# Optimization experiments

Measured on AMD Instinct MI355X. Metric: run time of the kernel, lower is better.

The kernel has to match this reference:

```python
import jax, jax.numpy as jnp
import numpy as np

B, L, D = 32, 2048, 512
MODES = 32
H = 1           # num_head
E = D // H      # per-head channels
KMA = 128       # moving_avg kernel
EPS = 1e-5


def setup_inputs() -> dict:
    key = jax.random.key(0)
    ks = jax.random.split(key, 12)
    scale = 1.0 / (D * D)
    lin = lambda k, fi, fo: jax.random.uniform(k, (fo, fi), jnp.float32, -1, 1) / np.sqrt(fi)
    return {
        "x": jax.random.normal(ks[0], (B, L, D), jnp.float32),
        "W_in": lin(ks[1], D, H * E),
        "b_in": jnp.zeros((H * E,), jnp.float32),
        "Wf_r": scale * jax.random.uniform(ks[2], (H, E, E, MODES), jnp.float32),
        "Wf_i": scale * jax.random.uniform(ks[3], (H, E, E, MODES), jnp.float32),
        "W_out": lin(ks[4], H * E, D),
        "b_out": jnp.zeros((D,), jnp.float32),
        "W_conv1": lin(ks[5], D, D),
        "W_conv2": lin(ks[6], D, D),
        "bn_gamma": jnp.ones((L,), jnp.float32),
        "bn_beta": jnp.zeros((L,), jnp.float32),
    }


def moving_average(x, k):
    # x: (b, l, c); replicate-pad front/end exactly as the torch module, then avg-pool k/stride 1
    front = jnp.repeat(x[:, :1, :], k - 1 - (k - 1) // 2, axis=1)
    end = jnp.repeat(x[:, -1:, :], (k - 1) // 2, axis=1)
    xp = jnp.concatenate([front, x, end], axis=1)          # (b, l+k-1, c)
    cs = jnp.cumsum(xp, axis=1)
    cs = jnp.concatenate([jnp.zeros_like(cs[:, :1]), cs], axis=1)
    return (cs[:, k:] - cs[:, :-k]) / k                    # (b, l, c)


def reference(x, W_in, b_in, Wf_r, Wf_i, W_out, b_out, W_conv1, W_conv2, bn_gamma, bn_beta):
    b, l, d = x.shape
    # in projection -> (b, l, h, e) -> (b, h, e, l)
    q = x @ W_in.T + b_in
    q = q.reshape(b, l, H, E).transpose(0, 2, 3, 1)
    # FourierBlock: rfft over time, keep lowest MODES modes, complex mix, irfft
    x_ft = jnp.fft.rfft(q, axis=-1)                        # (b, h, e, l//2+1)
    Wf = (Wf_r + 1j * Wf_i).astype(x_ft.dtype)             # (h, e, e, m)
    out_modes = jnp.einsum('bhim,hiom->bhom', x_ft[..., :MODES], Wf)
    out_ft = jnp.pad(out_modes, ((0, 0), (0, 0), (0, 0), (0, l // 2 + 1 - MODES)))
    fre = jnp.fft.irfft(out_ft, n=l, axis=-1)              # (b, h, e, l)
    # (b, h, e, l) -> (b, l, h*e), out projection (dropout is eval-mode identity)
    fre = fre.transpose(0, 3, 1, 2).reshape(b, l, H * E)
    fre = fre @ W_out.T + b_out
    xr = x + fre
    # series decomposition 1: keep residual
    xr = xr - moving_average(xr, KMA)
    # conv1x1 -> gelu -> conv1x1 (exact erf gelu, matching F.gelu default)
    y = jax.nn.gelu(jnp.einsum('bld,ed->ble', xr, W_conv1), approximate=False)
    y = jnp.einsum('bld,ed->ble', y, W_conv2)
    res = xr + y
    # BatchNorm1d(in_len): channel axis is the time axis, batch stats over (b, d)
    mean = res.mean(axis=(0, 2), keepdims=True)
    var = ((res - mean) ** 2).mean(axis=(0, 2), keepdims=True)
    out = bn_gamma[None, :, None] * (res - mean) / jnp.sqrt(var + EPS) + bn_beta[None, :, None]
    return out
```

## Files before the change

### kernel.cpp

```cpp
#include <hip/hip_runtime.h>
#include <hip/hip_bf16.h>
#include <math.h>

#define B_   32
#define L_   2048
#define D_   512
#define BLROWS (B_*L_)
#define NBIG ((size_t)BLROWS * D_)

typedef __hip_bfloat16 bf16;
using bf16x8 = __attribute__((ext_vector_type(8))) short;
using f32x4  = __attribute__((ext_vector_type(4))) float;

__device__ __forceinline__ unsigned short f2b(float f) {
  bf16 h = __float2bfloat16(f);
  return *reinterpret_cast<unsigned short*>(&h);
}
__device__ __forceinline__ float b2f(unsigned short u) {
  union { unsigned int i; float f; } c;
  c.i = ((unsigned int)u) << 16;
  return c.f;
}

__device__ __forceinline__ void gl_lds16(const void* g, void* l) {
  __builtin_amdgcn_global_load_lds(
      (const __attribute__((address_space(1))) void*)g,
      (__attribute__((address_space(3))) void*)l, 16, 0, 0);
}

__global__ __launch_bounds__(256) void f2bfK(const float4* __restrict__ src,
                                             ushort4* __restrict__ dst,
                                             size_t n4) {
  for (size_t i = (size_t)blockIdx.x * 256 + threadIdx.x; i < n4;
       i += (size_t)gridDim.x * 256) {
    float4 v = src[i];
    ushort4 o;
    o.x = f2b(v.x); o.y = f2b(v.y); o.z = f2b(v.z); o.w = f2b(v.w);
    dst[i] = o;
  }
}

__global__ __launch_bounds__(256) void genTwP(float* __restrict__ TwP) {
  int idx = blockIdx.x * 256 + threadIdx.x;
  int l = idx >> 6, rem = idx & 63, mg = rem >> 4, j = rem & 15;
  int m = mg * 8 + (j & 7);
  int r = (m * l) & (L_ - 1);
  float ang = (float)r * (6.283185307179586f / (float)L_);
  TwP[idx] = (j < 8) ? cosf(ang) : -sinf(ang);
}

__global__ __launch_bounds__(256) void genTbF(float* __restrict__ Tb) {
  int idx = blockIdx.x * 256 + threadIdx.x;
  int l = idx >> 6, j = idx & 63;
  int m = j >> 1;
  int r = (m * l) & (L_ - 1);
  float ang = (float)r * (6.283185307179586f / (float)L_);
  Tb[idx] = (j & 1) ? sinf(ang) : cosf(ang);
}

__global__ __launch_bounds__(256) void genTbDbf(const float* __restrict__ Tb,
                                                bf16* __restrict__ TbD) {
  int idx = blockIdx.x * 256 + threadIdx.x;
  int l = idx >> 6, j = idx & 63;
  float s = 0.f;
  for (int t = l - 64; t < l + 64; t++) {
    int cl = min(max(t, 0), L_ - 1);
    s += Tb[cl * 64 + j];
  }
  TbD[idx] = __float2bfloat16(Tb[idx] - s * (1.f / 128.f));
}

__global__ __launch_bounds__(256) void twWf2(const float* __restrict__ Wfr,
                                             const float* __restrict__ Wfi,
                                             bf16* __restrict__ Wcat2) {
  __shared__ __align__(16) bf16 st[256 * 72];
  const int t = threadIdx.x;
  const int i0 = blockIdx.x * 64, o0 = blockIdx.y * 8;
  const int arr = blockIdx.z;
  const float* src = arr ? Wfi : Wfr;
#pragma unroll
  for (int s8 = 0; s8 < 8; s8++) {
    unsigned short v[8];
#pragma unroll
    for (int ss = 0; ss < 8; ss++)
      v[ss] = f2b(src[(size_t)(i0 + s8 * 8 + ss) * 16384 + o0 * 32 + t]);
    int4 wv;
    wv.x = (int)v[0] | ((int)v[1] << 16);
    wv.y = (int)v[2] | ((int)v[3] << 16);
    wv.z = (int)v[4] | ((int)v[5] << 16);
    wv.w = (int)v[6] | ((int)v[7] << 16);
    *(int4*)&st[t * 72 + s8 * 8] = wv;
  }
  __syncthreads();
#pragma unroll
  for (int p = 0; p < 8; p++) {
    const int om = p * 32 + (t >> 3), c = t & 7;
    const int o = om >> 5, m = om & 31;
    int4 rv = *(const int4*)&st[om * 72 + c * 8];
    bf16* dst = Wcat2 + (size_t)m * 524288 + (size_t)(o0 + o) * 1024 +
                arr * 512 + i0 + c * 8;
    *(int4*)dst = rv;
  }
}

template <bool GELU, bool RESID, bool BIAS, bool OUTBF, bool RESBF, bool AFP32>
__global__ __launch_bounds__(256) void gemm_k64(
    const void* __restrict__ Av, const bf16* __restrict__ Wt,
    const float* __restrict__ bias, const void* __restrict__ resid,
    void* __restrict__ Cout, int M, int N, int K) {
  __shared__ __align__(16) bf16 As[2][128 * 64];
  __shared__ __align__(16) bf16 Bs[2][128 * 64];
  const int t = threadIdx.x;
  const int lane = t & 63;
  const int w = t >> 6, wr = w >> 1, wc = w & 1;

  const int id = blockIdx.x;
  const int xcd = id & 7, rest = id >> 3;
  const int cb = rest & 3, rg = rest >> 2;
  const int row0 = (rg * 8 + xcd) * 128, col0 = cb * 128;

  const bf16* Ab = (const bf16*)Av;
  const float* Af = (const float*)Av;

  f32x4 acc[4][4];
#pragma unroll
  for (int i = 0; i < 4; i++)
#pragma unroll
    for (int j = 0; j < 4; j++) acc[i][j] = (f32x4){0.f, 0.f, 0.f, 0.f};

  auto stage = [&](int buf, int k0) {
#pragma unroll
    for (int s = 0; s < 4; s++) {
      const int ci = s * 256 + t;
      const int row = ci >> 3;
      const int cg = ci & 7;
      const int pc = cg ^ (row & 7);
      if (AFP32) {
        const float* ax = Af + (size_t)(row0 + row) * K + k0 + cg * 8;
        float4 v0 = *(const float4*)(ax);
        float4 v1 = *(const float4*)(ax + 4);
        int4 wv;
        wv.x = (int)f2b(v0.x) | ((int)f2b(v0.y) << 16);
        wv.y = (int)f2b(v0.z) | ((int)f2b(v0.w) << 16);
        wv.z = (int)f2b(v1.x) | ((int)f2b(v1.y) << 16);
        wv.w = (int)f2b(v1.z) | ((int)f2b(v1.w) << 16);
        *(int4*)&As[buf][(size_t)(row * 8 + pc) * 8] = wv;
      } else {
        const int kqg = cg ^ (row & 7);
        bf16* dA = &As[buf][(size_t)(s * 256 + (t & ~63)) * 8];
        gl_lds16(Ab + (size_t)(row0 + row) * K + k0 + kqg * 8, dA);
      }
      {
        const int kqg = cg ^ (row & 7);
        bf16* dB = &Bs[buf][(size_t)(s * 256 + (t & ~63)) * 8];
        gl_lds16(Wt + (size_t)(col0 + row) * K + k0 + kqg * 8, dB);
      }
    }
  };

  stage(0, 0);
  int cur = 0;
  for (int k0 = 0; k0 < K; k0 += 64) {
    __syncthreads();
    if (k0 + 64 < K) stage(cur ^ 1, k0 + 64);
#pragma unroll
    for (int ks = 0; ks < 2; ks++) {
      const int c = ks * 4 + (lane >> 4);
      const int pc = c ^ (lane & 7);
      bf16x8 af[4], bg[4];
#pragma unroll
      for (int m = 0; m < 4; m++) {
        const int ra = wr * 64 + m * 16 + (lane & 15);
        af[m] = *reinterpret_cast<const bf16x8*>(&As[cur][(ra * 8 + pc) * 8]);
      }
#pragma unroll
      for (int n = 0; n < 4; n++) {
        const int rb = wc * 64 + n * 16 + (lane & 15);
        bg[n] = *reinterpret_cast<const bf16x8*>(&Bs[cur][(rb * 8 + pc) * 8]);
      }
#pragma unroll
      for (int n = 0; n < 4; n++)
#pragma unroll
        for (int m = 0; m < 4; m++)
          acc[n][m] = __builtin_amdgcn_mfma_f32_16x16x32_bf16(
              bg[n], af[m], acc[n][m], 0, 0, 0);
    }
    cur ^= 1;
  }

  float* Cf = (float*)Cout;
  ushort* Cb = (ushort*)Cout;
#pragma unroll
  for (int n = 0; n < 4; n++) {
    const int dbase = col0 + wc * 64 + n * 16 + ((lane >> 4) << 2);
    float4 bsv = {0.f, 0.f, 0.f, 0.f};
    if (BIAS) bsv = *(const float4*)(bias + dbase);
#pragma unroll
    for (int m = 0; m < 4; m++) {
      const size_t r = (size_t)row0 + wr * 64 + m * 16 + (lane & 15);
      float v[4];
#pragma unroll
      for (int j = 0; j < 4; j++) {
        float u = acc[n][m][j] + (BIAS ? (&bsv.x)[j] : 0.f);
        if (GELU) u = 0.5f * u * (1.0f + erff(u * 0.70710678118654752f));
        v[j] = u;
      }
      if (RESID) {
        if (RESBF) {
          ushort4 rv = *(const ushort4*)((const ushort*)resid + r * N + dbase);
          v[0] += b2f(rv.x); v[1] += b2f(rv.y);
          v[2] += b2f(rv.z); v[3] += b2f(rv.w);
        } else {
          float4 rv = *(const float4*)((const float*)resid + r * N + dbase);
          v[0] += rv.x; v[1] += rv.y; v[2] += rv.z; v[3] += rv.w;
        }
      }
      if (OUTBF) {
        ushort4 o = {f2b(v[0]), f2b(v[1]), f2b(v[2]), f2b(v[3])};
        *(ushort4*)(Cb + r * N + dbase) = o;
      } else {
        float4 o = {v[0], v[1], v[2], v[3]};
        *(float4*)(Cf + r * N + dbase) = o;
      }
    }
  }
}

__global__ __launch_bounds__(256) void gemmD(
    const bf16* __restrict__ TbD, const bf16* __restrict__ CCT,
    const ushort* __restrict__ u, ushort* __restrict__ xr) {
  __shared__ __align__(16) bf16 As[128 * 64];
  __shared__ __align__(16) bf16 Bs[128 * 64];
  const int t = threadIdx.x;
  const int lane = t & 63;
  const int wid = t >> 6, wr = wid >> 1, wc = wid & 1;
  const int row0 = blockIdx.x * 128, col0 = blockIdx.y * 128;
  const int b = blockIdx.z;
  const bf16* Bsrc = CCT + (size_t)b * 512 * 64;

  const int srow = t >> 3, schk = t & 7;
  const int wb16 = (t & ~63) * 8;
#pragma unroll
  for (int p = 0; p < 4; p++) {
    gl_lds16(TbD + (size_t)(row0 + srow + 32 * p) * 64 + schk * 8,
             &As[p * 2048 + wb16]);
    gl_lds16(Bsrc + (size_t)(col0 + srow + 32 * p) * 64 + schk * 8,
             &Bs[p * 2048 + wb16]);
  }
  __syncthreads();

  f32x4 acc[4][4];
#pragma unroll
  for (int i = 0; i < 4; i++)
#pragma unroll
    for (int j = 0; j < 4; j++) acc[i][j] = (f32x4){0.f, 0.f, 0.f, 0.f};

#pragma unroll
  for (int ks = 0; ks < 2; ks++) {
    bf16x8 af[4], bg[4];
#pragma unroll
    for (int m = 0; m < 4; m++)
      af[m] = *reinterpret_cast<const bf16x8*>(
          &As[(wr * 64 + m * 16 + (lane & 15)) * 64 + ks * 32 +
              (lane >> 4) * 8]);
#pragma unroll
    for (int n = 0; n < 4; n++)
      bg[n] = *reinterpret_cast<const bf16x8*>(
          &Bs[(wc * 64 + n * 16 + (lane & 15)) * 64 + ks * 32 +
              (lane >> 4) * 8]);
#pragma unroll
    for (int n = 0; n < 4; n++)
#pragma unroll
      for (int m = 0; m < 4; m++)
        acc[n][m] = __builtin_amdgcn_mfma_f32_16x16x32_bf16(bg[n], af[m],
                                                            acc[n][m], 0, 0, 0);
  }

#pragma unroll
  for (int n = 0; n < 4; n++) {
    const int dbase = col0 + wc * 64 + n * 16 + ((lane >> 4) << 2);
#pragma unroll
    for (int m = 0; m < 4; m++) {
      const int l = row0 + wr * 64 + m * 16 + (lane & 15);
      const size_t rg = ((size_t)b * L_ + l) * D_ + dbase;
      ushort4 uv = *(const ushort4*)(u + rg);
      ushort4 o;
      o.x = f2b(acc[n][m][0] + b2f(uv.x));
      o.y = f2b(acc[n][m][1] + b2f(uv.y));
      o.z = f2b(acc[n][m][2] + b2f(uv.z));
      o.w = f2b(acc[n][m][3] + b2f(uv.w));
      *(ushort4*)(xr + rg) = o;
    }
  }
}

template <bool BIAS, bool OUTBF, bool MGUARD, int EPI>
__global__ __launch_bounds__(256) void gemm_bt(
    const bf16* __restrict__ A, const bf16* __restrict__ Wt,
    const float* __restrict__ bias, void* __restrict__ Cout,
    int M, int N, int K, long batchA, long batchB, long batchC,
    int ldc, int coff) {
  __shared__ __align__(16) bf16 As[2][128 * 32];
  __shared__ __align__(16) bf16 Bs[2][128 * 32];
  const int t = threadIdx.x;
  const int lane = t & 63;
  const int wid = t >> 6, wr = wid >> 1, wc = wid & 1;
  const int row0 = blockIdx.x * 128, col0 = blockIdx.y * 128;
  const int zb = blockIdx.z;
  A += (size_t)zb * (size_t)batchA;
  Wt += (size_t)zb * (size_t)batchB;

  f32x4 acc[4][4];
#pragma unroll
  for (int i = 0; i < 4; i++)
#pragma unroll
    for (int j = 0; j < 4; j++) acc[i][j] = (f32x4){0.f, 0.f, 0.f, 0.f};

  const int srow = t >> 2, scq = t & 3;
  const int sa0 = MGUARD ? (srow & 31) : srow;
  const int sa1 = MGUARD ? (srow & 31) : (64 + srow);
  const int wbase = (t & ~63) * 8;

  auto stage = [&](int buf, int k0) {
    gl_lds16(A + (size_t)(row0 + sa0) * K + k0 + scq * 8, &As[buf][wbase]);
    gl_lds16(A + (size_t)(row0 + sa1) * K + k0 + scq * 8,
             &As[buf][2048 + wbase]);
    gl_lds16(Wt + (size_t)(col0 + srow) * K + k0 + scq * 8, &Bs[buf][wbase]);
    gl_lds16(Wt + (size_t)(col0 + 64 + srow) * K + k0 + scq * 8,
             &Bs[buf][2048 + wbase]);
  };

  stage(0, 0);
  int cur = 0;
  for (int k0 = 0; k0 < K; k0 += 32) {
    __syncthreads();
    if (k0 + 32 < K) stage(cur ^ 1, k0 + 32);
    bf16x8 af[4], bg[4];
#pragma unroll
    for (int m = 0; m < 4; m++)
      af[m] = *reinterpret_cast<const bf16x8*>(
          &As[cur][(wr * 64 + m * 16 + (lane & 15)) * 32 + (lane >> 4) * 8]);
#pragma unroll
    for (int n = 0; n < 4; n++)
      bg[n] = *reinterpret_cast<const bf16x8*>(
          &Bs[cur][(wc * 64 + n * 16 + (lane & 15)) * 32 + (lane >> 4) * 8]);
#pragma unroll
    for (int m = 0; m < 4; m++)
#pragma unroll
      for (int n = 0; n < 4; n++)
        acc[m][n] = __builtin_amdgcn_mfma_f32_16x16x32_bf16(af[m], bg[n],
                                                            acc[m][n], 0, 0, 0);
    cur ^= 1;
  }

  if (EPI == 3 || EPI == 4) {
    bf16* Cb = (bf16*)Cout;
#pragma unroll
    for (int n = 0; n < 4; n++) {
      int col = col0 + wc * 64 + n * 16 + (lane & 15);
#pragma unroll
      for (int m = 0; m < 4; m++) {
#pragma unroll
        for (int j = 0; j < 4; j++) {
          int row = row0 + wr * 64 + m * 16 + (lane >> 4) * 4 + j;
          int bb = row >> 5, mm = row & 31;
          float scale = (EPI == 3)
              ? ((mm == 0) ? (1.f / (float)L_) : (2.f / (float)L_))
              : (-2.f / (float)L_);
          Cb[((size_t)bb * 512 + col) * 64 + 2 * mm + (EPI == 4 ? 1 : 0)] =
              __float2bfloat16(acc[m][n][j] * scale);
        }
      }
    }
    return;
  }

  float* Cf = (float*)Cout;
  bf16* Cb = (bf16*)Cout;
  const size_t cbase = (size_t)zb * (size_t)batchC;
#pragma unroll
  for (int n = 0; n < 4; n++) {
    int col = col0 + wc * 64 + n * 16 + (lane & 15);
    float bs = 0.f;
    if (BIAS) bs = bias[col];
#pragma unroll
    for (int m = 0; m < 4; m++) {
#pragma unroll
      for (int j = 0; j < 4; j++) {
        int row = row0 + wr * 64 + m * 16 + (lane >> 4) * 4 + j;
        if (MGUARD && row >= M) continue;
        float v = acc[m][n][j] + bs;
        size_t idx = cbase + (size_t)row * ldc + coff + col;
        if (OUTBF) Cb[idx] = __float2bfloat16(v);
        else Cf[idx] = v;
      }
    }
  }
}

__global__ __launch_bounds__(256) void stageB(
    const bf16* __restrict__ q, const float* __restrict__ TwP,
    float* __restrict__ XFp_r, float* __restrict__ XFp_i) {
  __shared__ __align__(16) float Tls[4 * 128 * 16];
  const int b = blockIdx.x, ig = blockIdx.y, lc = blockIdx.z;
  const int t = threadIdx.x, lane = t & 63, mg = t >> 6;
  const int i0 = ig * 64;
  float ar[8], ai[8];
#pragma unroll
  for (int k = 0; k < 8; k++) { ar[k] = 0.f; ai[k] = 0.f; }
  float* TlsW = &Tls[mg * 2048];

  for (int h = 0; h < 2; h++) {
    const int hb = lc * 256 + h * 128;
#pragma unroll
    for (int s = 0; s < 8; s++) {
      int flat = s * 64 + lane;
      int l = flat >> 2, q4 = flat & 3;
      gl_lds16(TwP + ((size_t)(hb + l) * 4 + mg) * 16 + q4 * 4,
               TlsW + s * 256);
    }
    __syncthreads();
#pragma unroll 4
    for (int l = 0; l < 128; l++) {
      float qv = __bfloat162float(q[((size_t)b * L_ + hb + l) * D_ + i0 + lane]);
      const float* Tp = TlsW + l * 16;
      float4 c0 = *(const float4*)(Tp);
      float4 c1 = *(const float4*)(Tp + 4);
      float4 s0 = *(const float4*)(Tp + 8);
      float4 s1 = *(const float4*)(Tp + 12);
      ar[0] += qv * c0.x; ar[1] += qv * c0.y; ar[2] += qv * c0.z; ar[3] += qv * c0.w;
      ar[4] += qv * c1.x; ar[5] += qv * c1.y; ar[6] += qv * c1.z; ar[7] += qv * c1.w;
      ai[0] += qv * s0.x; ai[1] += qv * s0.y; ai[2] += qv * s0.z; ai[3] += qv * s0.w;
      ai[4] += qv * s1.x; ai[5] += qv * s1.y; ai[6] += qv * s1.z; ai[7] += qv * s1.w;
    }
    __syncthreads();
  }
  size_t base = (((size_t)lc * B_ + b) * D_ + i0 + lane) * 32 + mg * 8;
  float4 r0 = {ar[0], ar[1], ar[2], ar[3]}, r1 = {ar[4], ar[5], ar[6], ar[7]};
  float4 i0v = {ai[0], ai[1], ai[2], ai[3]}, i1v = {ai[4], ai[5], ai[6], ai[7]};
  *(float4*)(XFp_r + base) = r0;
  *(float4*)(XFp_r + base + 4) = r1;
  *(float4*)(XFp_i + base) = i0v;
  *(float4*)(XFp_i + base + 4) = i1v;
}

__global__ __launch_bounds__(256) void reduceXFT(
    const float* __restrict__ XFp_r, const float* __restrict__ XFp_i,
    bf16* __restrict__ Aneg, bf16* __restrict__ Aswap) {
  __shared__ float smr[64][33], smi[64][33];
  const int b = blockIdx.x, ic = blockIdx.y;
  const int i0 = ic * 64;
  const size_t CS = (size_t)B_ * D_ * 32;
#pragma unroll
  for (int s = 0; s < 8; s++) {
    int flat = s * 256 + threadIdx.x;
    int i = flat >> 5, m = flat & 31;
    size_t e = ((size_t)b * D_ + i0 + i) * 32 + m;
    float sr = 0.f, si = 0.f;
#pragma unroll
    for (int c = 0; c < 8; c++) { sr += XFp_r[c * CS + e]; si += XFp_i[c * CS + e]; }
    smr[i][m] = sr;
    smi[i][m] = si;
  }
  __syncthreads();
#pragma unroll
  for (int s = 0; s < 8; s++) {
    int flat = s * 256 + threadIdx.x;
    int m = flat >> 6, i = flat & 63;
    float sr = smr[i][m], si = smi[i][m];
    size_t base = ((size_t)m * B_ + b) * 1024;
    Aneg[base + i0 + i] = __float2bfloat16(sr);
    Aneg[base + 512 + i0 + i] = __float2bfloat16(-si);
    Aswap[base + i0 + i] = __float2bfloat16(si);
    Aswap[base + 512 + i0 + i] = __float2bfloat16(sr);
  }
}

__global__ __launch_bounds__(256) void stageE(const float* __restrict__ in,
                                              bf16* __restrict__ outbf) {
  const int b = blockIdx.x, dg = blockIdx.y, lc = blockIdx.z;
  const int d = dg * 256 + threadIdx.x;
  const float* col = in + (size_t)b * L_ * D_ + d;
  bf16* bcol = outbf + (size_t)b * L_ * D_ + d;
  const int l0 = lc * 128;
  float Wsum = 0.f;
  for (int s = l0 - 64; s < l0 + 64; s++) {
    int cl = min(max(s, 0), L_ - 1);
    Wsum += col[(size_t)cl * D_];
  }
  for (int l = l0; l < l0 + 128; l++) {
    float v = col[(size_t)l * D_];
    bcol[(size_t)l * D_] = __float2bfloat16(v - Wsum * (1.f / 128.f));
    int fa = min(l + 64, L_ - 1);
    int fb = max(l - 64, 0);
    Wsum += col[(size_t)fa * D_] - col[(size_t)fb * D_];
  }
}

__global__ __launch_bounds__(256) void bnStats(const ushort* __restrict__ res,
                                               float* __restrict__ meanb,
                                               float* __restrict__ rstdb) {
  const int l = blockIdx.x;
  const int t = threadIdx.x;
  float s = 0.f, s2 = 0.f;
  for (int b = 0; b < B_; b++) {
    const ushort* p = res + ((size_t)b * L_ + l) * D_ + 2 * t;
    ushort2 v2 = *(const ushort2*)p;
    float a = b2f(v2.x), c = b2f(v2.y);
    s += a + c;
    s2 += a * a + c * c;
  }
#pragma unroll
  for (int off = 32; off > 0; off >>= 1) {
    s += __shfl_down(s, off, 64);
    s2 += __shfl_down(s2, off, 64);
  }
  __shared__ float shs[4], shs2[4];
  int wid = t >> 6;
  if ((t & 63) == 0) { shs[wid] = s; shs2[wid] = s2; }
  __syncthreads();
  if (t == 0) {
    float S = shs[0] + shs[1] + shs[2] + shs[3];
    float S2 = shs2[0] + shs2[1] + shs2[2] + shs2[3];
    const float inv = 1.f / (float)(B_ * D_);
    float mean = S * inv;
    float var = S2 * inv - mean * mean;
    meanb[l] = mean;
    rstdb[l] = rsqrtf(var + 1e-5f);
  }
}

__global__ __launch_bounds__(256) void bnApply(
    const ushort* __restrict__ res, const float* __restrict__ gamma,
    const float* __restrict__ beta, const float* __restrict__ meanb,
    const float* __restrict__ rstdb, float* __restrict__ out) {
  size_t idx = (size_t)blockIdx.x * 256 + threadIdx.x;
  if (idx >= NBIG / 4) return;
  size_t e = idx * 4;
  int l = (int)((e >> 9) & (L_ - 1));
  ushort4 v = *(const ushort4*)(res + e);
  float m = meanb[l], rs = rstdb[l];
  float g = gamma[l] * rs, bt = beta[l];
  float4 o;
  o.x = (b2f(v.x) - m) * g + bt;
  o.y = (b2f(v.y) - m) * g + bt;
  o.z = (b2f(v.z) - m) * g + bt;
  o.w = (b2f(v.w) - m) * g + bt;
  *(float4*)(out + e) = o;
}

extern "C" void kernel_launch(void* const* d_in, const int* in_sizes, int n_in,
                              void* d_out, int out_size, void* d_ws,
                              size_t ws_size, hipStream_t stream) {
  const float* x      = (const float*)d_in[0];
  const float* W_in   = (const float*)d_in[1];
  const float* b_in   = (const float*)d_in[2];
  const float* Wf_r   = (const float*)d_in[3];
  const float* Wf_i   = (const float*)d_in[4];
  const float* W_out  = (const float*)d_in[5];
  const float* b_out  = (const float*)d_in[6];
  const float* W_c1   = (const float*)d_in[7];
  const float* W_c2   = (const float*)d_in[8];
  const float* gamma  = (const float*)d_in[9];
  const float* beta   = (const float*)d_in[10];
  float* outp = (float*)d_out;
  (void)b_out;

  float* f = (float*)d_ws;
  float* buf0 = f;
  bf16*  resbf = (bf16*)buf0;
  float* XFp_r = buf0;
  float* XFp_i = XFp_r + (size_t)8 * 524288;
  bf16*  Wcat2 = (bf16*)(XFp_i + (size_t)8 * 524288);
  bf16*  Woutbf= Wcat2 + (size_t)32 * 512 * 1024;
  bf16*  Aneg  = Woutbf + 262144;
  bf16*  Aswap = Aneg + 1048576;
  bf16*  OMr   = Aswap + 1048576;
  bf16*  OMi   = OMr + 524288;
  bf16*  CCT   = OMi + 524288;
  float* TwP   = f + NBIG;
  float* TbF   = TwP + 131072;
  bf16*  TbD   = (bf16*)(TbF + 131072);
  bf16*  Wibf  = TbD + 131072;
  bf16*  W1bf  = Wibf + 262144;
  bf16*  W2bf  = W1bf + 262144;
  float* meanb = (float*)(W2bf + 262144);
  float* rstdb = meanb + L_;

  bf16* qbf  = ((bf16*)d_out) + NBIG;
  bf16* ubf  = qbf;
  bf16* xrbf = (bf16*)d_out;
  bf16* y1bf = qbf;

  genTwP<<<512, 256, 0, stream>>>(TwP);
  genTbF<<<512, 256, 0, stream>>>(TbF);
  genTbDbf<<<512, 256, 0, stream>>>(TbF, TbD);
  f2bfK<<<256, 256, 0, stream>>>((const float4*)W_in, (ushort4*)Wibf, 65536);
  f2bfK<<<256, 256, 0, stream>>>((const float4*)W_c1, (ushort4*)W1bf, 65536);
  f2bfK<<<256, 256, 0, stream>>>((const float4*)W_c2, (ushort4*)W2bf, 65536);
  f2bfK<<<256, 256, 0, stream>>>((const float4*)W_out, (ushort4*)Woutbf, 65536);
  twWf2<<<dim3(8, 64, 2), 256, 0, stream>>>(Wf_r, Wf_i, Wcat2);

  gemm_k64<false, false, true, true, false, true><<<2048, 256, 0, stream>>>(
      x, Wibf, b_in, nullptr, qbf, BLROWS, D_, D_);

  stageB<<<dim3(B_, 8, 8), 256, 0, stream>>>(qbf, TwP, XFp_r, XFp_i);
  reduceXFT<<<dim3(B_, 8), 256, 0, stream>>>(XFp_r, XFp_i, Aneg, Aswap);

  gemm_bt<false, true, true, 0><<<dim3(1, 4, 32), 256, 0, stream>>>(
      Aneg, Wcat2, nullptr, OMr, 32, 512, 1024, 32768, 524288, 512, 16384, 0);
  gemm_bt<false, true, true, 0><<<dim3(1, 4, 32), 256, 0, stream>>>(
      Aswap, Wcat2, nullptr, OMi, 32, 512, 1024, 32768, 524288, 512, 16384, 0);

  gemm_bt<false, true, false, 3><<<dim3(8, 4, 1), 256, 0, stream>>>(
      OMr, Woutbf, nullptr, CCT, 1024, 512, 512, 0, 0, 0, 0, 0);
  gemm_bt<false, true, false, 4><<<dim3(8, 4, 1), 256, 0, stream>>>(
      OMi, Woutbf, nullptr, CCT, 1024, 512, 512, 0, 0, 0, 0, 0);

  stageE<<<dim3(B_, 2, 16), 256, 0, stream>>>(x, ubf);

  gemmD<<<dim3(16, 4, 32), 256, 0, stream>>>(TbD, CCT, (const ushort*)ubf,
                                             (ushort*)xrbf);

  gemm_k64<true, false, false, true, false, false><<<2048, 256, 0, stream>>>(
      xrbf, W1bf, nullptr, nullptr, y1bf, BLROWS, D_, D_);

  gemm_k64<false, true, false, true, true, false><<<2048, 256, 0, stream>>>(
      y1bf, W2bf, nullptr, xrbf, resbf, BLROWS, D_, D_);

  bnStats<<<L_, 256, 0, stream>>>((const ushort*)resbf, meanb, rstdb);
  bnApply<<<(NBIG / 4 + 255) / 256, 256, 0, stream>>>(
      (const ushort*)resbf, gamma, beta, meanb, rstdb, outp);
}
```

Baseline: 685.3 us.

## Fuse truncated DFT into input-projection GEMM epilogue via MFMA

The input projection GEMM no longer writes q to global memory. Its epilogue transposes the 128x128 output tile into swizzled LDS and multiplies it by a bf16 twiddle table with MFMA, producing per-block partial DFT coefficients for the 32 modes. This removes the scalar FP32 stageB kernel and the full q round trip through memory. The reduce kernel now sums 16 bf16 partials per batch. Storing both the twiddles and the partial sums in bf16 adds precision loss.

```diff
diff --git a/kernel.cpp b/kernel.cpp
--- a/kernel.cpp
+++ b/kernel.cpp
@@ -40,13 +40,13 @@
   }
 }
 
-__global__ __launch_bounds__(256) void genTwP(float* __restrict__ TwP) {
+__global__ __launch_bounds__(256) void genTwCS(bf16* __restrict__ TwCS) {
   int idx = blockIdx.x * 256 + threadIdx.x;
-  int l = idx >> 6, rem = idx & 63, mg = rem >> 4, j = rem & 15;
-  int m = mg * 8 + (j & 7);
+  int mrow = idx >> 11, l = idx & 2047;
+  int m = mrow & 31;
   int r = (m * l) & (L_ - 1);
   float ang = (float)r * (6.283185307179586f / (float)L_);
-  TwP[idx] = (j < 8) ? cosf(ang) : -sinf(ang);
+  TwCS[idx] = __float2bfloat16((mrow < 32) ? cosf(ang) : -sinf(ang));
 }
 
 __global__ __launch_bounds__(256) void genTbF(float* __restrict__ Tb) {
@@ -103,11 +103,13 @@
   }
 }
 
-template <bool GELU, bool RESID, bool BIAS, bool OUTBF, bool RESBF, bool AFP32>
+template <bool GELU, bool RESID, bool BIAS, bool OUTBF, bool RESBF, bool AFP32,
+          bool DFTE>
 __global__ __launch_bounds__(256) void gemm_k64(
     const void* __restrict__ Av, const bf16* __restrict__ Wt,
     const float* __restrict__ bias, const void* __restrict__ resid,
-    void* __restrict__ Cout, int M, int N, int K) {
+    void* __restrict__ Cout, int M, int N, int K,
+    const bf16* __restrict__ TwCS, bf16* __restrict__ Pdft) {
   __shared__ __align__(16) bf16 As[2][128 * 64];
   __shared__ __align__(16) bf16 Bs[2][128 * 64];
   const int t = threadIdx.x;
@@ -188,6 +190,69 @@
     cur ^= 1;
   }
 
+  if (DFTE) {
+    bf16* QT = (bf16*)As;
+    __syncthreads();
+#pragma unroll
+    for (int n = 0; n < 4; n++) {
+      const int ibase = wc * 64 + n * 16 + ((lane >> 4) << 2);
+      float4 bsv = *(const float4*)(bias + col0 + ibase);
+#pragma unroll
+      for (int m = 0; m < 4; m++) {
+        const int lloc = wr * 64 + m * 16 + (lane & 15);
+#pragma unroll
+        for (int j = 0; j < 4; j++) {
+          const int iloc = ibase + j;
+          float u = acc[n][m][j] + (&bsv.x)[j];
+          QT[iloc * 128 + (((lloc >> 3) ^ (iloc & 7)) << 3) + (lloc & 7)] =
+              __float2bfloat16(u);
+        }
+      }
+    }
+    __syncthreads();
+    const int bidx = row0 >> 11, lblk = (row0 >> 7) & 15;
+    const int l0g = row0 & 2047;
+    f32x4 accd[4][2];
+#pragma unroll
+    for (int mp = 0; mp < 4; mp++)
+#pragma unroll
+      for (int ip = 0; ip < 2; ip++) accd[mp][ip] = (f32x4){0.f,0.f,0.f,0.f};
+#pragma unroll
+    for (int kc = 0; kc < 4; kc++) {
+      bf16x8 bgt[4], afq[2];
+#pragma unroll
+      for (int mp = 0; mp < 4; mp++)
+        bgt[mp] = *reinterpret_cast<const bf16x8*>(
+            TwCS + (size_t)(mp * 16 + (lane & 15)) * 2048 + l0g + kc * 32 +
+            (lane >> 4) * 8);
+#pragma unroll
+      for (int ip = 0; ip < 2; ip++) {
+        const int iloc = (w * 2 + ip) * 16 + (lane & 15);
+        const int kchunk = kc * 4 + (lane >> 4);
+        const int pcq = kchunk ^ (iloc & 7);
+        afq[ip] = *reinterpret_cast<const bf16x8*>(&QT[iloc * 128 + pcq * 8]);
+      }
+#pragma unroll
+      for (int mp = 0; mp < 4; mp++)
+#pragma unroll
+        for (int ip = 0; ip < 2; ip++)
+          accd[mp][ip] = __builtin_amdgcn_mfma_f32_16x16x32_bf16(
+              bgt[mp], afq[ip], accd[mp][ip], 0, 0, 0);
+    }
+    bf16* Pb = Pdft + (size_t)(bidx * 16 + lblk) * 64 * 512;
+#pragma unroll
+    for (int mp = 0; mp < 4; mp++)
+#pragma unroll
+      for (int ip = 0; ip < 2; ip++)
+#pragma unroll
+        for (int j = 0; j < 4; j++) {
+          const int mrow = mp * 16 + ((lane >> 4) << 2) + j;
+          const int ig = col0 + (w * 2 + ip) * 16 + (lane & 15);
+          Pb[(size_t)mrow * 512 + ig] = __float2bfloat16(accd[mp][ip][j]);
+        }
+    return;
+  }
+
   float* Cf = (float*)Cout;
   ushort* Cb = (ushort*)Cout;
 #pragma unroll
@@ -398,81 +463,27 @@
   }
 }
 
-__global__ __launch_bounds__(256) void stageB(
-    const bf16* __restrict__ q, const float* __restrict__ TwP,
-    float* __restrict__ XFp_r, float* __restrict__ XFp_i) {
-  __shared__ __align__(16) float Tls[4 * 128 * 16];
-  const int b = blockIdx.x, ig = blockIdx.y, lc = blockIdx.z;
-  const int t = threadIdx.x, lane = t & 63, mg = t >> 6;
-  const int i0 = ig * 64;
-  float ar[8], ai[8];
-#pragma unroll
-  for (int k = 0; k < 8; k++) { ar[k] = 0.f; ai[k] = 0.f; }
-  float* TlsW = &Tls[mg * 2048];
-
-  for (int h = 0; h < 2; h++) {
-    const int hb = lc * 256 + h * 128;
-#pragma unroll
-    for (int s = 0; s < 8; s++) {
-      int flat = s * 64 + lane;
-      int l = flat >> 2, q4 = flat & 3;
-      gl_lds16(TwP + ((size_t)(hb + l) * 4 + mg) * 16 + q4 * 4,
-               TlsW + s * 256);
-    }
-    __syncthreads();
-#pragma unroll 4
-    for (int l = 0; l < 128; l++) {
-      float qv = __bfloat162float(q[((size_t)b * L_ + hb + l) * D_ + i0 + lane]);
-      const float* Tp = TlsW + l * 16;
-      float4 c0 = *(const float4*)(Tp);
-      float4 c1 = *(const float4*)(Tp + 4);
-      float4 s0 = *(const float4*)(Tp + 8);
-      float4 s1 = *(const float4*)(Tp + 12);
-      ar[0] += qv * c0.x; ar[1] += qv * c0.y; ar[2] += qv * c0.z; ar[3] += qv * c0.w;
-      ar[4] += qv * c1.x; ar[5] += qv * c1.y; ar[6] += qv * c1.z; ar[7] += qv * c1.w;
-      ai[0] += qv * s0.x; ai[1] += qv * s0.y; ai[2] += qv * s0.z; ai[3] += qv * s0.w;
-      ai[4] += qv * s1.x; ai[5] += qv * s1.y; ai[6] += qv * s1.z; ai[7] += qv * s1.w;
-    }
-    __syncthreads();
-  }
-  size_t base = (((size_t)lc * B_ + b) * D_ + i0 + lane) * 32 + mg * 8;
-  float4 r0 = {ar[0], ar[1], ar[2], ar[3]}, r1 = {ar[4], ar[5], ar[6], ar[7]};
-  float4 i0v = {ai[0], ai[1], ai[2], ai[3]}, i1v = {ai[4], ai[5], ai[6], ai[7]};
-  *(float4*)(XFp_r + base) = r0;
-  *(float4*)(XFp_r + base + 4) = r1;
-  *(float4*)(XFp_i + base) = i0v;
-  *(float4*)(XFp_i + base + 4) = i1v;
-}
-
 __global__ __launch_bounds__(256) void reduceXFT(
-    const float* __restrict__ XFp_r, const float* __restrict__ XFp_i,
+    const bf16* __restrict__ Pdft,
     bf16* __restrict__ Aneg, bf16* __restrict__ Aswap) {
-  __shared__ float smr[64][33], smi[64][33];
   const int b = blockIdx.x, ic = blockIdx.y;
   const int i0 = ic * 64;
-  const size_t CS = (size_t)B_ * D_ * 32;
-#pragma unroll
-  for (int s = 0; s < 8; s++) {
-    int flat = s * 256 + threadIdx.x;
-    int i = flat >> 5, m = flat & 31;
-    size_t e = ((size_t)b * D_ + i0 + i) * 32 + m;
-    float sr = 0.f, si = 0.f;
-#pragma unroll
-    for (int c = 0; c < 8; c++) { sr += XFp_r[c * CS + e]; si += XFp_i[c * CS + e]; }
-    smr[i][m] = sr;
-    smi[i][m] = si;
-  }
-  __syncthreads();
 #pragma unroll
   for (int s = 0; s < 8; s++) {
     int flat = s * 256 + threadIdx.x;
     int m = flat >> 6, i = flat & 63;
-    float sr = smr[i][m], si = smi[i][m];
-    size_t base = ((size_t)m * B_ + b) * 1024;
-    Aneg[base + i0 + i] = __float2bfloat16(sr);
-    Aneg[base + 512 + i0 + i] = __float2bfloat16(-si);
-    Aswap[base + i0 + i] = __float2bfloat16(si);
-    Aswap[base + 512 + i0 + i] = __float2bfloat16(sr);
+    float sr = 0.f, si = 0.f;
+#pragma unroll
+    for (int lb = 0; lb < 16; lb++) {
+      const bf16* base = Pdft + (size_t)(b * 16 + lb) * 64 * 512;
+      sr += b2f(*(const unsigned short*)&base[(size_t)m * 512 + i0 + i]);
+      si += b2f(*(const unsigned short*)&base[(size_t)(32 + m) * 512 + i0 + i]);
+    }
+    size_t ab = ((size_t)m * B_ + b) * 1024;
+    Aneg[ab + i0 + i] = __float2bfloat16(sr);
+    Aneg[ab + 512 + i0 + i] = __float2bfloat16(-si);
+    Aswap[ab + i0 + i] = __float2bfloat16(si);
+    Aswap[ab + 512 + i0 + i] = __float2bfloat16(sr);
   }
 }
 
@@ -569,17 +580,16 @@
   float* f = (float*)d_ws;
   float* buf0 = f;
   bf16*  resbf = (bf16*)buf0;
-  float* XFp_r = buf0;
-  float* XFp_i = XFp_r + (size_t)8 * 524288;
-  bf16*  Wcat2 = (bf16*)(XFp_i + (size_t)8 * 524288);
+  bf16*  Pdft  = (bf16*)buf0;
+  bf16*  Wcat2 = Pdft + (size_t)512 * 64 * 512;
   bf16*  Woutbf= Wcat2 + (size_t)32 * 512 * 1024;
   bf16*  Aneg  = Woutbf + 262144;
   bf16*  Aswap = Aneg + 1048576;
   bf16*  OMr   = Aswap + 1048576;
   bf16*  OMi   = OMr + 524288;
   bf16*  CCT   = OMi + 524288;
-  float* TwP   = f + NBIG;
-  float* TbF   = TwP + 131072;
+  bf16*  TwCS  = (bf16*)(f + NBIG);
+  float* TbF   = (float*)(TwCS + 131072);
   bf16*  TbD   = (bf16*)(TbF + 131072);
   bf16*  Wibf  = TbD + 131072;
   bf16*  W1bf  = Wibf + 262144;
@@ -587,12 +597,11 @@
   float* meanb = (float*)(W2bf + 262144);
   float* rstdb = meanb + L_;
 
-  bf16* qbf  = ((bf16*)d_out) + NBIG;
-  bf16* ubf  = qbf;
+  bf16* ubf  = ((bf16*)d_out) + NBIG;
   bf16* xrbf = (bf16*)d_out;
-  bf16* y1bf = qbf;
-
-  genTwP<<<512, 256, 0, stream>>>(TwP);
+  bf16* y1bf = ubf;
+
+  genTwCS<<<512, 256, 0, stream>>>(TwCS);
   genTbF<<<512, 256, 0, stream>>>(TbF);
   genTbDbf<<<512, 256, 0, stream>>>(TbF, TbD);
   f2bfK<<<256, 256, 0, stream>>>((const float4*)W_in, (ushort4*)Wibf, 65536);
@@ -601,11 +610,11 @@
   f2bfK<<<256, 256, 0, stream>>>((const float4*)W_out, (ushort4*)Woutbf, 65536);
   twWf2<<<dim3(8, 64, 2), 256, 0, stream>>>(Wf_r, Wf_i, Wcat2);
 
-  gemm_k64<false, false, true, true, false, true><<<2048, 256, 0, stream>>>(
-      x, Wibf, b_in, nullptr, qbf, BLROWS, D_, D_);
-
-  stageB<<<dim3(B_, 8, 8), 256, 0, stream>>>(qbf, TwP, XFp_r, XFp_i);
-  reduceXFT<<<dim3(B_, 8), 256, 0, stream>>>(XFp_r, XFp_i, Aneg, Aswap);
+  gemm_k64<false, false, true, false, false, true, true>
+      <<<2048, 256, 0, stream>>>(
+      x, Wibf, b_in, nullptr, nullptr, BLROWS, D_, D_, TwCS, Pdft);
+
+  reduceXFT<<<dim3(B_, 8), 256, 0, stream>>>(Pdft, Aneg, Aswap);
 
   gemm_bt<false, true, true, 0><<<dim3(1, 4, 32), 256, 0, stream>>>(
       Aneg, Wcat2, nullptr, OMr, 32, 512, 1024, 32768, 524288, 512, 16384, 0);
@@ -622,11 +631,13 @@
   gemmD<<<dim3(16, 4, 32), 256, 0, stream>>>(TbD, CCT, (const ushort*)ubf,
                                              (ushort*)xrbf);
 
-  gemm_k64<true, false, false, true, false, false><<<2048, 256, 0, stream>>>(
-      xrbf, W1bf, nullptr, nullptr, y1bf, BLROWS, D_, D_);
-
-  gemm_k64<false, true, false, true, true, false><<<2048, 256, 0, stream>>>(
-      y1bf, W2bf, nullptr, xrbf, resbf, BLROWS, D_, D_);
+  gemm_k64<true, false, false, true, false, false, false>
+      <<<2048, 256, 0, stream>>>(
+      xrbf, W1bf, nullptr, nullptr, y1bf, BLROWS, D_, D_, nullptr, nullptr);
+
+  gemm_k64<false, true, false, true, true, false, false>
+      <<<2048, 256, 0, stream>>>(
+      y1bf, W2bf, nullptr, xrbf, resbf, BLROWS, D_, D_, nullptr, nullptr);
 
   bnStats<<<L_, 256, 0, stream>>>((const ushort*)resbf, meanb, rstdb);
   bnApply<<<(NBIG / 4 + 255) / 256, 256, 0, stream>>>(
```

Measured after the change: 600.0 us. -12.5%, faster.
